# Optimization experiments

Measured on AMD Instinct MI355X. Metric: run time of the kernel, lower is better.

## Reference

```python
import jax, jax.numpy as jnp
import numpy as np

FLOOR = 1e-06
B, T, C = 64, 4096, 80


def _ema(x, w):
    """EMA a_t = w*x_t + (1-w)*a_{t-1}, a_{-1} = x[:,0], via parallel associative scan.
    x: [B,T,C], w: [C] (clipped to [0,1]). Returns [B,T,C].
    Note: with init = x[:,0], the first output is exactly x[:,0].
    """
    A = jnp.broadcast_to(1.0 - w, x.shape)          # decay per step
    b = w * x                                        # input injection per step
    # Fold the initial state into step 0: a_0 = w*x_0 + (1-w)*x_0 = x_0
    A = A.at[:, 0, :].set(0.0)
    b = b.at[:, 0, :].set(x[:, 0, :])

    def combine(c1, c2):
        A1, b1 = c1
        A2, b2 = c2
        return A1 * A2, A2 * b1 + b2

    _, ema = jax.lax.associative_scan(combine, (A, b), axis=1)
    return ema


def setup_inputs() -> dict:
    key = jax.random.key(0)
    k_in, = jax.random.split(key, 1)
    inputs = jax.random.uniform(k_in, (B, T, C), dtype=jnp.float32)  # non-negative energies
    alpha = jnp.full((C,), 0.96, dtype=jnp.float32)
    delta = jnp.full((C,), 2.0, dtype=jnp.float32)
    root = jnp.full((C,), 2.0, dtype=jnp.float32)
    smooth = jnp.full((C,), 0.04, dtype=jnp.float32)
    return {"inputs": inputs, "alpha": alpha, "delta": delta, "root": root, "smooth": smooth}


def reference(inputs, alpha, delta, root, smooth):
    w = jnp.clip(smooth, 0.0, 1.0)
    a = jnp.minimum(alpha, 1.0)
    r = jnp.maximum(root, 1.0)
    ema_smoother = _ema(inputs, w)                       # [B,T,C]
    one_over_root = 1.0 / r                              # [C]
    out = (inputs / (FLOOR + ema_smoother) ** a + delta) ** one_over_root - delta ** one_over_root
    return out
```

## Files before the change

### kernel.cpp

```cpp
#include <hip/hip_runtime.h>

#define FLOOR_EPS 1e-6f

typedef float f32x4 __attribute__((ext_vector_type(4)));

constexpr int Bn     = 64;
constexpr int Tn     = 4096;
constexpr int Cn     = 80;
constexpr int G      = Cn / 4;
constexpr int P      = 16;
constexpr int SLAB   = Tn / P;
constexpr int KC     = 16;
constexpr int CH     = SLAB / KC;
constexpr int NT     = KC * G;
constexpr int NCHUNK = Tn / CH;
constexpr int TOT    = Bn * NCHUNK * G;

__device__ __forceinline__ void nt_store4(float4* p, float a, float b,
                                          float c, float d) {
    f32x4 v = {a, b, c, d};
    __builtin_nontemporal_store(v, (f32x4*)p);
}

__global__ __launch_bounds__(NT, 5)
void pcen_slabsum_kernel(const float* __restrict__ x,
                         const float* __restrict__ smooth,
                         float4* __restrict__ states)
{
    __shared__ float4 sc[2][KC][G];

    const int p  = blockIdx.x % P;
    const int b  = blockIdx.x / P;
    const int t  = threadIdx.x;
    const int g  = t % G;
    const int kc = t / G;

    const float4 smv = ((const float4*)smooth)[g];
    float w0 = fminf(fmaxf(smv.x, 0.f), 1.f), w1 = fminf(fmaxf(smv.y, 0.f), 1.f);
    float w2 = fminf(fmaxf(smv.z, 0.f), 1.f), w3 = fminf(fmaxf(smv.w, 0.f), 1.f);
    float d0 = 1.f - w0, d1 = 1.f - w1, d2 = 1.f - w2, d3 = 1.f - w3;

    float q0 = d0 * d0, q1 = d1 * d1, q2 = d2 * d2, q3 = d3 * d3;
    q0 *= q0; q1 *= q1; q2 *= q2; q3 *= q3;
    q0 *= q0; q1 *= q1; q2 *= q2; q3 *= q3;
    q0 *= q0; q1 *= q1; q2 *= q2; q3 *= q3;

    const size_t rowbase = ((size_t)b * Tn + (size_t)p * SLAB + (size_t)kc * CH) * G + g;
    const float4* px = (const float4*)x + rowbase;

    const bool fc = (p == 0) && (kc == 0);
    float e0, e1, e2, e3;
    if (fc) { float4 v = px[0]; e0 = v.x; e1 = v.y; e2 = v.z; e3 = v.w; }
    else    { e0 = 0.f; e1 = 0.f; e2 = 0.f; e3 = 0.f; }
    #pragma unroll
    for (int u = 0; u < CH; ++u) {
        float4 v = px[(size_t)u * G];
        e0 = fmaf(d0, e0, w0 * v.x);
        e1 = fmaf(d1, e1, w1 * v.y);
        e2 = fmaf(d2, e2, w2 * v.z);
        e3 = fmaf(d3, e3, w3 * v.w);
    }
    sc[0][kc][g] = make_float4(e0, e1, e2, e3);
    __syncthreads();

    float W0 = q0, W1 = q1, W2 = q2, W3 = q3;
    int src = 0;
    #pragma unroll
    for (int off = 1; off < KC; off <<= 1) {
        float4 v = sc[src][kc][g];
        if (kc >= off) {
            float4 u4 = sc[src][kc - off][g];
            v.x = fmaf(W0, u4.x, v.x);
            v.y = fmaf(W1, u4.y, v.y);
            v.z = fmaf(W2, u4.z, v.z);
            v.w = fmaf(W3, u4.w, v.w);
        }
        sc[src ^ 1][kc][g] = v;
        __syncthreads();
        src ^= 1;
        W0 *= W0; W1 *= W1; W2 *= W2; W3 *= W3;
    }

    states[(size_t)blockIdx.x * NT + t] = sc[src][kc][g];
}

__global__ __launch_bounds__(256)
void pcen_out_kernel(const float* __restrict__ x,
                     const float* __restrict__ alpha,
                     const float* __restrict__ delta,
                     const float* __restrict__ root,
                     const float* __restrict__ smooth,
                     const float4* __restrict__ states,
                     float* __restrict__ out)
{
    const int tid = blockIdx.x * blockDim.x + threadIdx.x;
    if (tid >= TOT) return;
    const int g = tid % G;
    const int k = (tid / G) % NCHUNK;
    const int b = tid / (G * NCHUNK);
    const int p  = k >> 4;
    const int kc = k & 15;

    const float4 smv = ((const float4*)smooth)[g];
    float w0 = fminf(fmaxf(smv.x, 0.f), 1.f), w1 = fminf(fmaxf(smv.y, 0.f), 1.f);
    float w2 = fminf(fmaxf(smv.z, 0.f), 1.f), w3 = fminf(fmaxf(smv.w, 0.f), 1.f);
    float d0 = 1.f - w0, d1 = 1.f - w1, d2 = 1.f - w2, d3 = 1.f - w3;

    float q0 = d0 * d0, q1 = d1 * d1, q2 = d2 * d2, q3 = d3 * d3;
    q0 *= q0; q1 *= q1; q2 *= q2; q3 *= q3;
    q0 *= q0; q1 *= q1; q2 *= q2; q3 *= q3;
    q0 *= q0; q1 *= q1; q2 *= q2; q3 *= q3;
    float W0 = q0, W1 = q1, W2 = q2, W3 = q3;
    W0 *= W0; W1 *= W1; W2 *= W2; W3 *= W3;
    W0 *= W0; W1 *= W1; W2 *= W2; W3 *= W3;
    W0 *= W0; W1 *= W1; W2 *= W2; W3 *= W3;
    W0 *= W0; W1 *= W1; W2 *= W2; W3 *= W3;

    float S0 = 0.f, S1 = 0.f, S2 = 0.f, S3 = 0.f;
    const size_t rowchunk = (size_t)b * NCHUNK;
    for (int q = 0; q < p; ++q) {
        float4 sq = states[(rowchunk + (size_t)q * KC + (KC - 1)) * G + g];
        S0 = fmaf(W0, S0, sq.x);
        S1 = fmaf(W1, S1, sq.y);
        S2 = fmaf(W2, S2, sq.z);
        S3 = fmaf(W3, S3, sq.w);
    }

    float m0, m1, m2, m3;
    if (kc == 0) {
        m0 = S0; m1 = S1; m2 = S2; m3 = S3;
    } else {
        float4 ex = states[(size_t)tid - G];
        float k0 = 1.f, k1 = 1.f, k2 = 1.f, k3 = 1.f;
        float b0 = q0, b1 = q1, b2 = q2, b3 = q3;
        int kk = kc;
        #pragma unroll
        for (int bit = 0; bit < 4; ++bit) {
            if (kk & 1) { k0 *= b0; k1 *= b1; k2 *= b2; k3 *= b3; }
            b0 *= b0; b1 *= b1; b2 *= b2; b3 *= b3;
            kk >>= 1;
        }
        m0 = fmaf(k0, S0, ex.x);
        m1 = fmaf(k1, S1, ex.y);
        m2 = fmaf(k2, S2, ex.z);
        m3 = fmaf(k3, S3, ex.w);
    }

    const size_t rowbase = ((size_t)b * Tn + (size_t)k * CH) * G + g;
    const float4* px = (const float4*)x + rowbase;
    float4* po = (float4*)out + rowbase;

    if (k == 0) { float4 v = px[0]; m0 = v.x; m1 = v.y; m2 = v.z; m3 = v.w; }

    const float4 alv = ((const float4*)alpha)[g];
    const float4 dlv = ((const float4*)delta)[g];
    const float4 rov = ((const float4*)root)[g];
    float nega[4], invr[4], dl[4], sub[4];
    {
        float as[4] = {alv.x, alv.y, alv.z, alv.w};
        float rs[4] = {rov.x, rov.y, rov.z, rov.w};
        dl[0] = dlv.x; dl[1] = dlv.y; dl[2] = dlv.z; dl[3] = dlv.w;
        #pragma unroll
        for (int j = 0; j < 4; ++j) {
            nega[j] = -fminf(as[j], 1.f);
            invr[j] = 1.f / fmaxf(rs[j], 1.f);
            sub[j]  = __expf(invr[j] * __logf(dl[j]));
        }
    }
    const bool all_sqrt = (invr[0] == 0.5f) & (invr[1] == 0.5f) &
                          (invr[2] == 0.5f) & (invr[3] == 0.5f);

    if (all_sqrt) {
        #pragma unroll
        for (int u = 0; u < CH; ++u) {
            float4 xv = px[(size_t)u * G];
            m0 = fmaf(d0, m0, w0 * xv.x);
            m1 = fmaf(d1, m1, w1 * xv.y);
            m2 = fmaf(d2, m2, w2 * xv.z);
            m3 = fmaf(d3, m3, w3 * xv.w);
            nt_store4(&po[(size_t)u * G],
                sqrtf(fmaf(xv.x, __expf(nega[0] * __logf(FLOOR_EPS + m0)), dl[0])) - sub[0],
                sqrtf(fmaf(xv.y, __expf(nega[1] * __logf(FLOOR_EPS + m1)), dl[1])) - sub[1],
                sqrtf(fmaf(xv.z, __expf(nega[2] * __logf(FLOOR_EPS + m2)), dl[2])) - sub[2],
                sqrtf(fmaf(xv.w, __expf(nega[3] * __logf(FLOOR_EPS + m3)), dl[3])) - sub[3]);
        }
    } else {
        float w[4] = {w0, w1, w2, w3}, dc[4] = {d0, d1, d2, d3};
        float mm[4] = {m0, m1, m2, m3};
        #pragma unroll
        for (int u = 0; u < CH; ++u) {
            float4 xv = px[(size_t)u * G];
            float xv4[4] = {xv.x, xv.y, xv.z, xv.w};
            float os[4];
            #pragma unroll
            for (int j = 0; j < 4; ++j) {
                mm[j]   = fmaf(dc[j], mm[j], w[j] * xv4[j]);
                float pw = __expf(nega[j] * __logf(FLOOR_EPS + mm[j]));
                float v  = fmaf(xv4[j], pw, dl[j]);
                os[j]    = __expf(invr[j] * __logf(v)) - sub[j];
            }
            nt_store4(&po[(size_t)u * G], os[0], os[1], os[2], os[3]);
        }
    }
}

extern "C" void kernel_launch(void* const* d_in, const int* in_sizes, int n_in,
                              void* d_out, int out_size, void* d_ws, size_t ws_size,
                              hipStream_t stream) {
    const float* x      = (const float*)d_in[0];
    const float* alpha  = (const float*)d_in[1];
    const float* delta  = (const float*)d_in[2];
    const float* root   = (const float*)d_in[3];
    const float* smooth = (const float*)d_in[4];
    float* out = (float*)d_out;

    float4* states = (float4*)d_ws;

    pcen_slabsum_kernel<<<Bn * P, NT, 0, stream>>>(x, smooth, states);

    int block = 256;
    int gridB = (TOT + block - 1) / block;
    pcen_out_kernel<<<gridB, block, 0, stream>>>(x, alpha, delta, root, smooth,
                                                 states, out);
}
```

Baseline: 173.7 us.

## Replace serial cross-slab carry loop with block-level shared-memory scan in output kernel

The output kernel now uses the same block shape as the slab-sum kernel: one block per (batch, slab) with KC×G threads. Each block loads the 16 slab-end states into shared memory and runs a log-step parallel scan to get the carry-in for its slab. Previously each thread walked a serial loop over up to 15 earlier slabs through global memory. The occupancy hint changes from 5 to 6 on both kernels, and the extra syncs and redundant per-block scans are the cost of this.

```diff
diff --git a/kernel.cpp b/kernel.cpp
--- a/kernel.cpp
+++ b/kernel.cpp
@@ -14,7 +14,6 @@
 constexpr int CH     = SLAB / KC;
 constexpr int NT     = KC * G;
 constexpr int NCHUNK = Tn / CH;
-constexpr int TOT    = Bn * NCHUNK * G;
 
 __device__ __forceinline__ void nt_store4(float4* p, float a, float b,
                                           float c, float d) {
@@ -22,7 +21,7 @@
     __builtin_nontemporal_store(v, (f32x4*)p);
 }
 
-__global__ __launch_bounds__(NT, 5)
+__global__ __launch_bounds__(NT, 6)
 void pcen_slabsum_kernel(const float* __restrict__ x,
                          const float* __restrict__ smooth,
                          float4* __restrict__ states)
@@ -84,7 +83,7 @@
     states[(size_t)blockIdx.x * NT + t] = sc[src][kc][g];
 }
 
-__global__ __launch_bounds__(256)
+__global__ __launch_bounds__(NT, 6)
 void pcen_out_kernel(const float* __restrict__ x,
                      const float* __restrict__ alpha,
                      const float* __restrict__ delta,
@@ -93,13 +92,13 @@
                      const float4* __restrict__ states,
                      float* __restrict__ out)
 {
-    const int tid = blockIdx.x * blockDim.x + threadIdx.x;
-    if (tid >= TOT) return;
-    const int g = tid % G;
-    const int k = (tid / G) % NCHUNK;
-    const int b = tid / (G * NCHUNK);
-    const int p  = k >> 4;
-    const int kc = k & 15;
+    __shared__ float4 sS[2][KC][G];
+
+    const int p  = blockIdx.x % P;
+    const int b  = blockIdx.x / P;
+    const int t  = threadIdx.x;
+    const int g  = t % G;
+    const int kc = t / G;
 
     const float4 smv = ((const float4*)smooth)[g];
     float w0 = fminf(fmaxf(smv.x, 0.f), 1.f), w1 = fminf(fmaxf(smv.y, 0.f), 1.f);
@@ -110,27 +109,46 @@
     q0 *= q0; q1 *= q1; q2 *= q2; q3 *= q3;
     q0 *= q0; q1 *= q1; q2 *= q2; q3 *= q3;
     q0 *= q0; q1 *= q1; q2 *= q2; q3 *= q3;
-    float W0 = q0, W1 = q1, W2 = q2, W3 = q3;
-    W0 *= W0; W1 *= W1; W2 *= W2; W3 *= W3;
-    W0 *= W0; W1 *= W1; W2 *= W2; W3 *= W3;
-    W0 *= W0; W1 *= W1; W2 *= W2; W3 *= W3;
-    W0 *= W0; W1 *= W1; W2 *= W2; W3 *= W3;
-
-    float S0 = 0.f, S1 = 0.f, S2 = 0.f, S3 = 0.f;
-    const size_t rowchunk = (size_t)b * NCHUNK;
-    for (int q = 0; q < p; ++q) {
-        float4 sq = states[(rowchunk + (size_t)q * KC + (KC - 1)) * G + g];
-        S0 = fmaf(W0, S0, sq.x);
-        S1 = fmaf(W1, S1, sq.y);
-        S2 = fmaf(W2, S2, sq.z);
-        S3 = fmaf(W3, S3, sq.w);
-    }
-
+
+    sS[0][kc][g] = states[((size_t)b * NCHUNK + kc * KC + (KC - 1)) * G + g];
+    __syncthreads();
+
+    float V0 = q0, V1 = q1, V2 = q2, V3 = q3;
+    V0 *= V0; V1 *= V1; V2 *= V2; V3 *= V3;
+    V0 *= V0; V1 *= V1; V2 *= V2; V3 *= V3;
+    V0 *= V0; V1 *= V1; V2 *= V2; V3 *= V3;
+    V0 *= V0; V1 *= V1; V2 *= V2; V3 *= V3;
+    int src = 0;
+    #pragma unroll
+    for (int off = 1; off < KC; off <<= 1) {
+        float4 v = sS[src][kc][g];
+        if (kc >= off) {
+            float4 u4 = sS[src][kc - off][g];
+            v.x = fmaf(V0, u4.x, v.x);
+            v.y = fmaf(V1, u4.y, v.y);
+            v.z = fmaf(V2, u4.z, v.z);
+            v.w = fmaf(V3, u4.w, v.w);
+        }
+        sS[src ^ 1][kc][g] = v;
+        __syncthreads();
+        src ^= 1;
+        V0 *= V0; V1 *= V1; V2 *= V2; V3 *= V3;
+    }
+
+    const size_t sidx = ((size_t)b * NCHUNK + (size_t)p * KC + kc) * G + g;
+    const size_t rowbase = ((size_t)b * Tn + ((size_t)p * KC + kc) * CH) * G + g;
+    const float4* px = (const float4*)x + rowbase;
+
+    float s0 = 0.f, s1 = 0.f, s2 = 0.f, s3 = 0.f;
+    if (p > 0) {
+        float4 Sg = sS[src][p - 1][g];
+        s0 = Sg.x; s1 = Sg.y; s2 = Sg.z; s3 = Sg.w;
+    }
     float m0, m1, m2, m3;
     if (kc == 0) {
-        m0 = S0; m1 = S1; m2 = S2; m3 = S3;
+        m0 = s0; m1 = s1; m2 = s2; m3 = s3;
     } else {
-        float4 ex = states[(size_t)tid - G];
+        float4 ex = states[sidx - G];
         float k0 = 1.f, k1 = 1.f, k2 = 1.f, k3 = 1.f;
         float b0 = q0, b1 = q1, b2 = q2, b3 = q3;
         int kk = kc;
@@ -140,17 +158,15 @@
             b0 *= b0; b1 *= b1; b2 *= b2; b3 *= b3;
             kk >>= 1;
         }
-        m0 = fmaf(k0, S0, ex.x);
-        m1 = fmaf(k1, S1, ex.y);
-        m2 = fmaf(k2, S2, ex.z);
-        m3 = fmaf(k3, S3, ex.w);
-    }
-
-    const size_t rowbase = ((size_t)b * Tn + (size_t)k * CH) * G + g;
-    const float4* px = (const float4*)x + rowbase;
-    float4* po = (float4*)out + rowbase;
-
-    if (k == 0) { float4 v = px[0]; m0 = v.x; m1 = v.y; m2 = v.z; m3 = v.w; }
+        m0 = fmaf(k0, s0, ex.x);
+        m1 = fmaf(k1, s1, ex.y);
+        m2 = fmaf(k2, s2, ex.z);
+        m3 = fmaf(k3, s3, ex.w);
+    }
+    if ((p == 0) && (kc == 0)) {
+        float4 v = px[0];
+        m0 = v.x; m1 = v.y; m2 = v.z; m3 = v.w;
+    }
 
     const float4 alv = ((const float4*)alpha)[g];
     const float4 dlv = ((const float4*)delta)[g];
@@ -169,6 +185,8 @@
     }
     const bool all_sqrt = (invr[0] == 0.5f) & (invr[1] == 0.5f) &
                           (invr[2] == 0.5f) & (invr[3] == 0.5f);
+
+    float4* po = (float4*)out + rowbase;
 
     if (all_sqrt) {
         #pragma unroll
@@ -217,9 +235,6 @@
     float4* states = (float4*)d_ws;
 
     pcen_slabsum_kernel<<<Bn * P, NT, 0, stream>>>(x, smooth, states);
-
-    int block = 256;
-    int gridB = (TOT + block - 1) / block;
-    pcen_out_kernel<<<gridB, block, 0, stream>>>(x, alpha, delta, root, smooth,
-                                                 states, out);
-}
+    pcen_out_kernel<<<Bn * P, NT, 0, stream>>>(x, alpha, delta, root, smooth,
+                                               states, out);
+}
```

Result: no change. 171.9 us, median of 2 (-1.0%).
